# Kernel optimization log

Hardware: AMD Instinct MI355X
Metric: run time of the kernel (lower is better)

## Reference

```python
import math
import jax, jax.numpy as jnp
import numpy as np

N_EXPERTS = 8
CAP_FACTOR = 1.25
D_MODEL = 1024
D_FF = 4096
B, T = 8, 2048


def setup_inputs() -> dict:
    key = jax.random.key(0)
    k1, k2, k3, k4 = jax.random.split(key, 4)
    hidden = jax.random.normal(k1, (B, T, D_MODEL), dtype=jnp.float32)
    # router: Linear(d_model, n_experts, bias=False), init std=0.01; store as (D, E)
    router_w = jax.random.normal(k2, (D_MODEL, N_EXPERTS), dtype=jnp.float32) * 0.01
    # per-expert MLP weights stacked: W1 (E, D, F), W2 (E, F, D)
    s1 = 1.0 / math.sqrt(D_MODEL)
    s2 = 1.0 / math.sqrt(D_FF)
    W1 = jax.random.uniform(k3, (N_EXPERTS, D_MODEL, D_FF), dtype=jnp.float32, minval=-s1, maxval=s1)
    W2 = jax.random.uniform(k4, (N_EXPERTS, D_FF, D_MODEL), dtype=jnp.float32, minval=-s2, maxval=s2)
    return {"hidden": hidden, "router_w": router_w, "W1": W1, "W2": W2}


def reference(hidden, router_w, W1, W2):
    Bb, Tt, D = hidden.shape
    N = Bb * Tt
    E = router_w.shape[1]
    capacity = min(int(math.ceil(CAP_FACTOR * N / E)), N)

    hidden_flat = hidden.reshape(N, D)
    logits = hidden_flat @ router_w                 # (N, E)
    router_probs = jax.nn.softmax(logits, axis=-1)  # (N, E)

    scores = router_probs.T                         # (E, N)
    weights, indices = jax.lax.top_k(scores, capacity)  # (E, C) each

    # gather tokens per expert: (E, C, D)
    expert_in = hidden_flat[indices]
    h = jnp.einsum('ecd,edf->ecf', expert_in, W1)
    h = jax.nn.gelu(h, approximate=False)           # torch nn.GELU default (erf)
    expert_out = jnp.einsum('ecf,efd->ecd', h, W2)  # (E, C, D)
    contrib = weights[..., None] * expert_out       # (E, C, D)

    output = jnp.zeros((N, D), dtype=hidden.dtype)
    output = output.at[indices.reshape(-1)].add(contrib.reshape(-1, D))
    output = output.reshape(Bb, Tt, D)

    eps = 1e-8
    entropy = -(router_probs * jnp.log(router_probs + eps)).sum(-1)
    aux_loss = -entropy.mean()
    return output, aux_loss
```

## Files before the change

### kernel.cpp

```cpp
#include <hip/hip_runtime.h>
#include <hip/hip_bf16.h>
#include <math.h>

#define NTOK 16384
#define DM 1024
#define DFF 4096
#define NEXP 8
#define CAP 2560

typedef __bf16 bf16;
typedef float f32x4 __attribute__((ext_vector_type(4)));
typedef bf16 bf16x8 __attribute__((ext_vector_type(8)));
typedef bf16 bf16x4 __attribute__((ext_vector_type(4)));

#define OFF_PROBS 0ull
#define OFF_IDX   524288ull
#define OFF_WTS   606208ull
#define OFF_W1T   688128ull
#define OFF_W2T   67796992ull
#define OFF_X     134905856ull
#define OFF_ENT   OFF_X
#define OFF_H     176848896ull
#define WS_MIN    197820416ull
#define WS_FUSED  344621056ull

__device__ __forceinline__ void gl16(const bf16* g, const bf16* l) {
  __builtin_amdgcn_global_load_lds((const __attribute__((address_space(1))) void*)g,
                                   (__attribute__((address_space(3))) void*)l, 16, 0, 0);
}

__device__ __forceinline__ float gelu_f(float x) {
  float u = 1.5957691216057308f * (x + 0.044715f * x * x * x);
  return x * __builtin_amdgcn_rcpf(1.f + __expf(-u));
}

__global__ __launch_bounds__(256) void k_transpose_cvt(const float* __restrict__ src,
                                                       bf16* __restrict__ dst, int R, int C) {
  __shared__ float tile[64][69];
  int e = blockIdx.z;
  src += (size_t)e * R * C;
  dst += (size_t)e * R * C;
  int c0 = blockIdx.x * 64, r0 = blockIdx.y * 64;
  int t = threadIdx.x;
  int tr = t >> 4, tc4 = (t & 15) * 4;
#pragma unroll
  for (int i = 0; i < 4; i++) {
    int r = tr + i * 16;
    float4 v = *(const float4*)(src + (size_t)(r0 + r) * C + c0 + tc4);
    tile[r][tc4] = v.x; tile[r][tc4 + 1] = v.y; tile[r][tc4 + 2] = v.z; tile[r][tc4 + 3] = v.w;
  }
  __syncthreads();
#pragma unroll
  for (int i = 0; i < 4; i++) {
    int orr = tr + i * 16;
    bf16x4 o = {(bf16)tile[tc4][orr], (bf16)tile[tc4 + 1][orr],
                (bf16)tile[tc4 + 2][orr], (bf16)tile[tc4 + 3][orr]};
    *(bf16x4*)(dst + (size_t)(c0 + orr) * R + r0 + tc4) = o;
  }
}

__global__ __launch_bounds__(256) void k_router(const float* __restrict__ hidden,
                                                const float* __restrict__ rw,
                                                float* __restrict__ probsT,
                                                float* __restrict__ entPart) {
  __shared__ float went[4];
  int wv = threadIdx.x >> 6, lane = threadIdx.x & 63;
  int token = blockIdx.x * 4 + wv;
  float acc[NEXP];
#pragma unroll
  for (int e = 0; e < NEXP; e++) acc[e] = 0.f;
  const float* hp = hidden + (size_t)token * DM;
  for (int d = lane; d < DM; d += 64) {
    float h = hp[d];
#pragma unroll
    for (int e = 0; e < NEXP; e++) acc[e] = fmaf(h, rw[d * NEXP + e], acc[e]);
  }
#pragma unroll
  for (int e = 0; e < NEXP; e++) {
    float v = acc[e];
#pragma unroll
    for (int s = 1; s < 64; s <<= 1) v += __shfl_xor(v, s);
    acc[e] = v;
  }
  float mx = acc[0];
#pragma unroll
  for (int e = 1; e < NEXP; e++) mx = fmaxf(mx, acc[e]);
  float p[NEXP], s = 0.f;
#pragma unroll
  for (int e = 0; e < NEXP; e++) { p[e] = expf(acc[e] - mx); s += p[e]; }
  float inv = 1.f / s;
  float ent = 0.f;
#pragma unroll
  for (int e = 0; e < NEXP; e++) { p[e] *= inv; ent += p[e] * logf(p[e] + 1e-8f); }
  if (lane < NEXP) probsT[(size_t)lane * NTOK + token] = p[lane];
  if (lane == 0) went[wv] = ent;
  __syncthreads();
  if (threadIdx.x == 0) entPart[blockIdx.x] = went[0] + went[1] + went[2] + went[3];
}

__global__ __launch_bounds__(256) void k_aux(const float* __restrict__ part, float* __restrict__ outAux) {
  __shared__ float s[256];
  int t = threadIdx.x;
  float v = 0.f;
#pragma unroll
  for (int i = 0; i < 16; i++) v += part[i * 256 + t];
  s[t] = v;
  __syncthreads();
  for (int st = 128; st > 0; st >>= 1) {
    if (t < st) s[t] += s[t + st];
    __syncthreads();
  }
  if (t == 0) outAux[0] = s[0] * (1.f / (float)NTOK);
}

__global__ __launch_bounds__(1024) void k_topk(const float* __restrict__ probsT,
                                               int* __restrict__ idx,
                                               float* __restrict__ wts) {
  int e = blockIdx.x;
  const float* row = probsT + (size_t)e * NTOK;
  int t = threadIdx.x;
  unsigned u[16];
#pragma unroll
  for (int j = 0; j < 16; j++) u[j] = __float_as_uint(row[j * 1024 + t]);
  __shared__ int wred[16];
  __shared__ int bc;
  __shared__ int cnt_gt, cnt_eq;
  __shared__ int eqbuf[2048];
  int lane = t & 63, wv = t >> 6;
  unsigned prefix = 0;
  for (int bit = 30; bit >= 0; bit--) {
    unsigned cand = prefix | (1u << bit);
    int c = 0;
#pragma unroll
    for (int j = 0; j < 16; j++) c += (u[j] >= cand) ? 1 : 0;
#pragma unroll
    for (int s = 1; s < 64; s <<= 1) c += __shfl_xor(c, s);
    if (lane == 0) wred[wv] = c;
    __syncthreads();
    if (t == 0) { int tot = 0; for (int k = 0; k < 16; k++) tot += wred[k]; bc = tot; }
    __syncthreads();
    if (bc >= CAP) prefix = cand;
  }
  unsigned vC = prefix;
  if (t == 0) { cnt_gt = 0; cnt_eq = 0; }
  __syncthreads();
#pragma unroll
  for (int j = 0; j < 16; j++) {
    int i = j * 1024 + t;
    if (u[j] > vC) {
      int p = atomicAdd(&cnt_gt, 1);
      idx[e * CAP + p] = i;
      wts[e * CAP + p] = __uint_as_float(u[j]);
    } else if (u[j] == vC) {
      int p = atomicAdd(&cnt_eq, 1);
      if (p < 2048) eqbuf[p] = i;
    }
  }
  __syncthreads();
  int m = cnt_gt;
  int ne = cnt_eq > 2048 ? 2048 : cnt_eq;
  int needed = CAP - m;
  for (int j = t; j < ne; j += 1024) {
    int my = eqbuf[j];
    int rank = 0;
    for (int k = 0; k < ne; k++) rank += (eqbuf[k] < my) ? 1 : 0;
    if (rank < needed) {
      idx[e * CAP + m + rank] = my;
      wts[e * CAP + m + rank] = __uint_as_float(vC);
    }
  }
}

__global__ void k_gather(const float* __restrict__ hidden, const int* __restrict__ idx,
                         bf16* __restrict__ X) {
  int ec = blockIdx.x;
  int token = idx[ec];
  const float4* src = (const float4*)(hidden + (size_t)token * DM);
  bf16* dstrow = X + (size_t)ec * DM;
  int t = threadIdx.x;
  float4 v = src[t];
  bf16x4 o = {(bf16)v.x, (bf16)v.y, (bf16)v.z, (bf16)v.w};
  *(bf16x4*)(dstrow + t * 4) = o;
}

template <int EPI>
__global__ __launch_bounds__(256) void k_gemm128(
    const bf16* __restrict__ Ab, const bf16* __restrict__ Bb,
    bf16* __restrict__ Hb, const int* __restrict__ idxb, const float* __restrict__ wtsb,
    float* __restrict__ outb, int serialE) {
  constexpr int KD = (EPI == 0) ? DM : DFF;
  constexpr int NT = (EPI == 0) ? 16 : 32;

  __shared__ bf16 As[128 * 64];
  __shared__ bf16 Bs[128 * 64];

  int e, j;
  if (serialE >= 0) { e = serialE; j = blockIdx.x; }
  else { e = blockIdx.x & 7; j = blockIdx.x >> 3; }
  int bx = j % 20, jr = j / 20;
  int m0 = bx * 128, n0, k0;
  if constexpr (EPI == 0) { n0 = jr * 128; k0 = 0; }
  else { n0 = (jr & 7) * 128; k0 = (jr >> 3) * 2048; }

  const bf16* A = Ab + (size_t)e * ((size_t)CAP * KD) + (size_t)m0 * KD;
  const bf16* B = Bb + (size_t)e * ((size_t)DFF * DM) + (size_t)n0 * KD;

  int t = threadIdx.x, lane = t & 63, wv = t >> 6;
  int wm = wv >> 1, wn = wv & 1;
  int l3 = lane >> 3, l7 = lane & 7;
  int cswz = (l7 ^ l3) * 8;

  f32x4 acc[4][4];
#pragma unroll
  for (int m = 0; m < 4; m++)
#pragma unroll
    for (int n = 0; n < 4; n++) acc[m][n] = (f32x4){0.f, 0.f, 0.f, 0.f};

  const bf16* gA0 = A + (size_t)(wv * 32 + l3) * KD + cswz;
  const bf16* gB0 = B + (size_t)(wv * 32 + l3) * KD + cswz;
  bf16* lA0 = As + wv * 2048 + lane * 8;
  bf16* lB0 = Bs + wv * 2048 + lane * 8;

  for (int kt = 0; kt < NT; kt++) {
    int ke = k0 + kt * 64;
#pragma unroll
    for (int jj = 0; jj < 4; jj++) {
      gl16(gA0 + (size_t)jj * 8 * KD + ke, lA0 + jj * 512);
      gl16(gB0 + (size_t)jj * 8 * KD + ke, lB0 + jj * 512);
    }
    __syncthreads();
#pragma unroll
    for (int kk = 0; kk < 2; kk++) {
      int kslot = kk * 4 + (lane >> 4);
      int slt = (kslot ^ l7) * 16;
      bf16x8 af[4], bfm[4];
#pragma unroll
      for (int m = 0; m < 4; m++) {
        int rr = wm * 64 + m * 16 + (lane & 15);
        af[m] = *(const bf16x8*)((const char*)As + rr * 128 + slt);
      }
#pragma unroll
      for (int n = 0; n < 4; n++) {
        int rr = wn * 64 + n * 16 + (lane & 15);
        bfm[n] = *(const bf16x8*)((const char*)Bs + rr * 128 + slt);
      }
#pragma unroll
      for (int m = 0; m < 4; m++)
#pragma unroll
        for (int n = 0; n < 4; n++)
          acc[m][n] = __builtin_amdgcn_mfma_f32_16x16x32_bf16(af[m], bfm[n], acc[m][n], 0, 0, 0);
    }
    __syncthreads();
  }

  int cl = lane & 15, rg = (lane >> 4) * 4;
  if constexpr (EPI == 0) {
    bf16* He = Hb + (size_t)e * CAP * DFF;
#pragma unroll
    for (int m = 0; m < 4; m++) {
      int rowg = m0 + wm * 64 + m * 16 + rg;
#pragma unroll
      for (int n = 0; n < 4; n++) {
        int col = n0 + wn * 64 + n * 16 + cl;
#pragma unroll
        for (int rr = 0; rr < 4; rr++)
          He[(size_t)(rowg + rr) * DFF + col] = (bf16)gelu_f(acc[m][n][rr]);
      }
    }
  } else {
    const int* idxE = idxb + e * CAP;
    const float* wtsE = wtsb + e * CAP;
#pragma unroll
    for (int m = 0; m < 4; m++) {
      int rowg = m0 + wm * 64 + m * 16 + rg;
#pragma unroll
      for (int rr = 0; rr < 4; rr++) {
        int c = rowg + rr;
        int token = idxE[c];
        float w = wtsE[c];
        float* op = outb + (size_t)token * DM + n0 + wn * 64 + cl;
#pragma unroll
        for (int n = 0; n < 4; n++) atomicAdd(op + n * 16, w * acc[m][n][rr]);
      }
    }
  }
}

extern "C" void kernel_launch(void* const* d_in, const int* in_sizes, int n_in,
                              void* d_out, int out_size, void* d_ws, size_t ws_size,
                              hipStream_t stream) {
  const float* hidden = (const float*)d_in[0];
  const float* router_w = (const float*)d_in[1];
  const float* W1 = (const float*)d_in[2];
  const float* W2 = (const float*)d_in[3];
  float* out = (float*)d_out;
  if (ws_size < WS_MIN) return;

  char* ws = (char*)d_ws;
  float* probsT = (float*)(ws + OFF_PROBS);
  int* idxb = (int*)(ws + OFF_IDX);
  float* wtsb = (float*)(ws + OFF_WTS);
  bf16* W1T = (bf16*)(ws + OFF_W1T);
  bf16* W2T = (bf16*)(ws + OFF_W2T);
  bf16* Xall = (bf16*)(ws + OFF_X);
  float* entPart = (float*)(ws + OFF_ENT);
  bf16* Hbuf = (bf16*)(ws + OFF_H);

  hipMemsetAsync(d_out, 0, (size_t)out_size * sizeof(float), stream);

  k_transpose_cvt<<<dim3(DFF / 64, DM / 64, NEXP), 256, 0, stream>>>(W1, W1T, DM, DFF);
  k_transpose_cvt<<<dim3(DM / 64, DFF / 64, NEXP), 256, 0, stream>>>(W2, W2T, DFF, DM);

  k_router<<<NTOK / 4, 256, 0, stream>>>(hidden, router_w, probsT, entPart);
  k_aux<<<1, 256, 0, stream>>>(entPart, out + (size_t)NTOK * DM);
  k_topk<<<NEXP, 1024, 0, stream>>>(probsT, idxb, wtsb);
  k_gather<<<NEXP * CAP, 256, 0, stream>>>(hidden, idxb, Xall);

  if (ws_size >= WS_FUSED) {
    k_gemm128<0><<<NEXP * 20 * 32, 256, 0, stream>>>(Xall, W1T, Hbuf, nullptr, nullptr, nullptr, -1);
    k_gemm128<1><<<NEXP * 20 * 16, 256, 0, stream>>>(Hbuf, W2T, nullptr, idxb, wtsb, out, -1);
  } else {
    for (int e = 0; e < NEXP; e++) {
      bf16* Hadj = Hbuf - (size_t)e * CAP * DFF;
      k_gemm128<0><<<20 * 32, 256, 0, stream>>>(Xall, W1T, Hadj, nullptr, nullptr, nullptr, e);
      k_gemm128<1><<<20 * 16, 256, 0, stream>>>(Hadj, W2T, nullptr, idxb, wtsb, out, e);
    }
  }
}
```

Baseline: 661.6 us.

## Double-buffer second expert GEMM and drop split-K atomics

The second expert GEMM moves to a dedicated kernel that double-buffers LDS tiles, issuing the next tile's global-to-LDS loads before computing the current one and managing vmcnt/lgkmcnt waits explicitly. It also drops the split-K over DFF, so each block covers the full K=4096 and does half as many atomic adds to the output. The trade-off is half as many blocks (less parallelism), double the LDS use, which may lower occupancy, and a longer serial K loop per block.

After: 617.7 us. 6.6% less time.

```diff
diff --git a/kernel.cpp b/kernel.cpp
--- a/kernel.cpp
+++ b/kernel.cpp
@@ -27,6 +27,14 @@
 __device__ __forceinline__ void gl16(const bf16* g, const bf16* l) {
   __builtin_amdgcn_global_load_lds((const __attribute__((address_space(1))) void*)g,
                                    (__attribute__((address_space(3))) void*)l, 16, 0, 0);
+}
+
+__device__ __forceinline__ bf16x8 ldsrd16(const bf16* a) {
+  bf16x8 d;
+  asm volatile("ds_read_b128 %0, %1"
+               : "=v"(d)
+               : "v"((const __attribute__((address_space(3))) bf16*)a));
+  return d;
 }
 
 __device__ __forceinline__ float gelu_f(float x) {
@@ -183,13 +191,11 @@
   *(bf16x4*)(dstrow + t * 4) = o;
 }
 
-template <int EPI>
 __global__ __launch_bounds__(256) void k_gemm128(
     const bf16* __restrict__ Ab, const bf16* __restrict__ Bb,
-    bf16* __restrict__ Hb, const int* __restrict__ idxb, const float* __restrict__ wtsb,
-    float* __restrict__ outb, int serialE) {
-  constexpr int KD = (EPI == 0) ? DM : DFF;
-  constexpr int NT = (EPI == 0) ? 16 : 32;
+    bf16* __restrict__ Hb, int serialE) {
+  constexpr int KD = DM;
+  constexpr int NT = 16;
 
   __shared__ bf16 As[128 * 64];
   __shared__ bf16 Bs[128 * 64];
@@ -198,9 +204,7 @@
   if (serialE >= 0) { e = serialE; j = blockIdx.x; }
   else { e = blockIdx.x & 7; j = blockIdx.x >> 3; }
   int bx = j % 20, jr = j / 20;
-  int m0 = bx * 128, n0, k0;
-  if constexpr (EPI == 0) { n0 = jr * 128; k0 = 0; }
-  else { n0 = (jr & 7) * 128; k0 = (jr >> 3) * 2048; }
+  int m0 = bx * 128, n0 = jr * 128;
 
   const bf16* A = Ab + (size_t)e * ((size_t)CAP * KD) + (size_t)m0 * KD;
   const bf16* B = Bb + (size_t)e * ((size_t)DFF * DM) + (size_t)n0 * KD;
@@ -222,7 +226,7 @@
   bf16* lB0 = Bs + wv * 2048 + lane * 8;
 
   for (int kt = 0; kt < NT; kt++) {
-    int ke = k0 + kt * 64;
+    int ke = kt * 64;
 #pragma unroll
     for (int jj = 0; jj < 4; jj++) {
       gl16(gA0 + (size_t)jj * 8 * KD + ke, lA0 + jj * 512);
@@ -254,34 +258,118 @@
   }
 
   int cl = lane & 15, rg = (lane >> 4) * 4;
-  if constexpr (EPI == 0) {
-    bf16* He = Hb + (size_t)e * CAP * DFF;
-#pragma unroll
-    for (int m = 0; m < 4; m++) {
-      int rowg = m0 + wm * 64 + m * 16 + rg;
+  bf16* He = Hb + (size_t)e * CAP * DFF;
+#pragma unroll
+  for (int m = 0; m < 4; m++) {
+    int rowg = m0 + wm * 64 + m * 16 + rg;
+#pragma unroll
+    for (int n = 0; n < 4; n++) {
+      int col = n0 + wn * 64 + n * 16 + cl;
+#pragma unroll
+      for (int rr = 0; rr < 4; rr++)
+        He[(size_t)(rowg + rr) * DFF + col] = (bf16)gelu_f(acc[m][n][rr]);
+    }
+  }
+}
+
+__global__ __launch_bounds__(256) void k_gemm2ph(
+    const bf16* __restrict__ Hb, const bf16* __restrict__ Bb,
+    const int* __restrict__ idxb, const float* __restrict__ wtsb,
+    float* __restrict__ outb, int serialE) {
+  constexpr int KD = DFF;
+  constexpr int NT = 64;
+
+  __shared__ bf16 As[2][128 * 64];
+  __shared__ bf16 Bs[2][128 * 64];
+
+  int e, j;
+  if (serialE >= 0) { e = serialE; j = blockIdx.x; }
+  else { e = blockIdx.x & 7; j = blockIdx.x >> 3; }
+  int bx = j % 20, by = j / 20;
+  int m0 = bx * 128, n0 = by * 128;
+
+  const bf16* A = Hb + (size_t)e * CAP * DFF + (size_t)m0 * KD;
+  const bf16* B = Bb + (size_t)e * DM * DFF + (size_t)n0 * KD;
+
+  int t = threadIdx.x, lane = t & 63, wv = t >> 6;
+  int wm = wv >> 1, wn = wv & 1;
+  int l3 = lane >> 3, l7 = lane & 7;
+  int cswz = (l7 ^ l3) * 8;
+
+  const bf16* gA0 = A + (size_t)(wv * 32 + l3) * KD + cswz;
+  const bf16* gB0 = B + (size_t)(wv * 32 + l3) * KD + cswz;
+
+  f32x4 acc[4][4];
+#pragma unroll
+  for (int m = 0; m < 4; m++)
+#pragma unroll
+    for (int n = 0; n < 4; n++) acc[m][n] = (f32x4){0.f, 0.f, 0.f, 0.f};
+
+  auto STAGE = [&](int buf, int ke) {
+    bf16* lA = &As[buf][wv * 2048 + lane * 8];
+    bf16* lB = &Bs[buf][wv * 2048 + lane * 8];
+#pragma unroll
+    for (int jj = 0; jj < 4; jj++) {
+      gl16(gA0 + (size_t)jj * 8 * KD + ke, lA + jj * 512);
+      gl16(gB0 + (size_t)jj * 8 * KD + ke, lB + jj * 512);
+    }
+  };
+
+  STAGE(0, 0);
+
+  for (int kt = 0; kt < NT; kt++) {
+    int cur = kt & 1;
+    if (kt < NT - 1) {
+      STAGE(cur ^ 1, (kt + 1) * 64);
+      asm volatile("s_waitcnt vmcnt(8)");
+    } else {
+      asm volatile("s_waitcnt vmcnt(0)");
+    }
+    __builtin_amdgcn_s_barrier();
+
+    bf16x8 af[4][2], bfm[4][2];
+#pragma unroll
+    for (int kk = 0; kk < 2; kk++) {
+      int kslot = kk * 4 + (lane >> 4);
+      int slt = (kslot ^ l7) * 16;
+#pragma unroll
+      for (int m = 0; m < 4; m++) {
+        int rr = wm * 64 + m * 16 + (lane & 15);
+        af[m][kk] = ldsrd16((const bf16*)((const char*)&As[cur][0] + rr * 128 + slt));
+      }
 #pragma unroll
       for (int n = 0; n < 4; n++) {
-        int col = n0 + wn * 64 + n * 16 + cl;
-#pragma unroll
-        for (int rr = 0; rr < 4; rr++)
-          He[(size_t)(rowg + rr) * DFF + col] = (bf16)gelu_f(acc[m][n][rr]);
+        int rr = wn * 64 + n * 16 + (lane & 15);
+        bfm[n][kk] = ldsrd16((const bf16*)((const char*)&Bs[cur][0] + rr * 128 + slt));
       }
     }
-  } else {
-    const int* idxE = idxb + e * CAP;
-    const float* wtsE = wtsb + e * CAP;
-#pragma unroll
-    for (int m = 0; m < 4; m++) {
-      int rowg = m0 + wm * 64 + m * 16 + rg;
-#pragma unroll
-      for (int rr = 0; rr < 4; rr++) {
-        int c = rowg + rr;
-        int token = idxE[c];
-        float w = wtsE[c];
-        float* op = outb + (size_t)token * DM + n0 + wn * 64 + cl;
-#pragma unroll
-        for (int n = 0; n < 4; n++) atomicAdd(op + n * 16, w * acc[m][n][rr]);
-      }
+    asm volatile("s_waitcnt lgkmcnt(0)");
+    __builtin_amdgcn_sched_barrier(0);
+    __builtin_amdgcn_s_barrier();
+
+#pragma unroll
+    for (int kk = 0; kk < 2; kk++)
+#pragma unroll
+      for (int m = 0; m < 4; m++)
+#pragma unroll
+        for (int n = 0; n < 4; n++)
+          acc[m][n] = __builtin_amdgcn_mfma_f32_16x16x32_bf16(af[m][kk], bfm[n][kk], acc[m][n], 0, 0, 0);
+  }
+
+  int cl = lane & 15, rg = (lane >> 4) * 4;
+  const int* idxE = idxb + e * CAP;
+  const float* wtsE = wtsb + e * CAP;
+#pragma unroll
+  for (int m = 0; m < 4; m++) {
+    int rowg = m0 + wm * 64 + m * 16 + rg;
+#pragma unroll
+    for (int rr = 0; rr < 4; rr++) {
+      int c = rowg + rr;
+      int token = idxE[c];
+      float w = wtsE[c];
+      float* op = outb + (size_t)token * DM + n0 + wn * 64 + cl;
+#pragma unroll
+      for (int n = 0; n < 4; n++) atomicAdd(op + n * 16, w * acc[m][n][rr]);
     }
   }
 }
@@ -317,13 +405,13 @@
   k_gather<<<NEXP * CAP, 256, 0, stream>>>(hidden, idxb, Xall);
 
   if (ws_size >= WS_FUSED) {
-    k_gemm128<0><<<NEXP * 20 * 32, 256, 0, stream>>>(Xall, W1T, Hbuf, nullptr, nullptr, nullptr, -1);
-    k_gemm128<1><<<NEXP * 20 * 16, 256, 0, stream>>>(Hbuf, W2T, nullptr, idxb, wtsb, out, -1);
+    k_gemm128<<<NEXP * 20 * 32, 256, 0, stream>>>(Xall, W1T, Hbuf, -1);
+    k_gemm2ph<<<NEXP * 20 * 8, 256, 0, stream>>>(Hbuf, W2T, idxb, wtsb, out, -1);
   } else {
     for (int e = 0; e < NEXP; e++) {
       bf16* Hadj = Hbuf - (size_t)e * CAP * DFF;
-      k_gemm128<0><<<20 * 32, 256, 0, stream>>>(Xall, W1T, Hadj, nullptr, nullptr, nullptr, e);
-      k_gemm128<1><<<20 * 16, 256, 0, stream>>>(Hadj, W2T, nullptr, idxb, wtsb, out, e);
-    }
-  }
-}
+      k_gemm128<<<20 * 32, 256, 0, stream>>>(Xall, W1T, Hadj, e);
+      k_gemm2ph<<<20 * 8, 256, 0, stream>>>(Hadj, W2T, idxb, wtsb, out, e);
+    }
+  }
+}
```

## Rewrite expert GEMMs with 256-row tiles, double-buffered LDS and 512 threads

Applied to the files above, without the earlier changes.

Replaces the 128x128 single-buffered GEMM with a templated kernel using 256x256 (first GEMM) and 256x128 (second GEMM) tiles, 8 waves per block, and double-buffered LDS so global-to-LDS loads for the next k-step overlap MFMA work on the current one. LDS reads use inline ds_read_b128 with explicit waitcnt and sched_barrier to control instruction ordering. The second GEMM drops the split-K over DFF, so its atomics are no longer shared across two K halves, but it has far fewer blocks (640). The larger tiles raise register and LDS pressure (64 KB or 48 KB of LDS) and lower occupancy.

Result: faster. 590.6 us (-10.7%).

```diff
diff --git a/kernel.cpp b/kernel.cpp
--- a/kernel.cpp
+++ b/kernel.cpp
@@ -29,6 +29,14 @@
                                    (__attribute__((address_space(3))) void*)l, 16, 0, 0);
 }
 
+__device__ __forceinline__ bf16x8 ldsrd16(const bf16* a) {
+  bf16x8 d;
+  asm volatile("ds_read_b128 %0, %1"
+               : "=v"(d)
+               : "v"((const __attribute__((address_space(3))) bf16*)a));
+  return d;
+}
+
 __device__ __forceinline__ float gelu_f(float x) {
   float u = 1.5957691216057308f * (x + 0.044715f * x * x * x);
   return x * __builtin_amdgcn_rcpf(1.f + __expf(-u));
@@ -183,85 +191,134 @@
   *(bf16x4*)(dstrow + t * 4) = o;
 }
 
-template <int EPI>
-__global__ __launch_bounds__(256) void k_gemm128(
+template <int EPI, int BM, int BN, int WMW, int WNW, int NT, int KD>
+__global__ __launch_bounds__(512) void k_gemm2ph(
     const bf16* __restrict__ Ab, const bf16* __restrict__ Bb,
     bf16* __restrict__ Hb, const int* __restrict__ idxb, const float* __restrict__ wtsb,
     float* __restrict__ outb, int serialE) {
-  constexpr int KD = (EPI == 0) ? DM : DFF;
-  constexpr int NT = (EPI == 0) ? 16 : 32;
-
-  __shared__ bf16 As[128 * 64];
-  __shared__ bf16 Bs[128 * 64];
+  constexpr int MF = (BM / WMW) / 16;
+  constexpr int NF = (BN / WNW) / 16;
+  constexpr int CA = BM / 8;
+  constexpr int CB = BN / 8;
+  constexpr int S = (CA + CB) / 8;
+  constexpr bool SPLIT = (MF + NF) <= 8;
+
+  __shared__ bf16 As[2][BM * 64];
+  __shared__ bf16 Bs[2][BN * 64];
 
   int e, j;
   if (serialE >= 0) { e = serialE; j = blockIdx.x; }
   else { e = blockIdx.x & 7; j = blockIdx.x >> 3; }
-  int bx = j % 20, jr = j / 20;
-  int m0 = bx * 128, n0, k0;
-  if constexpr (EPI == 0) { n0 = jr * 128; k0 = 0; }
-  else { n0 = (jr & 7) * 128; k0 = (jr >> 3) * 2048; }
-
-  const bf16* A = Ab + (size_t)e * ((size_t)CAP * KD) + (size_t)m0 * KD;
-  const bf16* B = Bb + (size_t)e * ((size_t)DFF * DM) + (size_t)n0 * KD;
+  int m0 = (j % 10) * 256;
+  int n0 = (j / 10) * BN;
+
+  const bf16* A = Ab + (size_t)e * CAP * KD + (size_t)m0 * KD;
+  const bf16* B = Bb + (size_t)e * DFF * DM + (size_t)n0 * KD;
 
   int t = threadIdx.x, lane = t & 63, wv = t >> 6;
-  int wm = wv >> 1, wn = wv & 1;
-  int l3 = lane >> 3, l7 = lane & 7;
+  int wm = wv / WNW, wn = wv % WNW;
+  int l3 = lane >> 3, l7 = lane & 7, l15 = lane & 15, khalf = lane >> 4;
   int cswz = (l7 ^ l3) * 8;
 
-  f32x4 acc[4][4];
-#pragma unroll
-  for (int m = 0; m < 4; m++)
-#pragma unroll
-    for (int n = 0; n < 4; n++) acc[m][n] = (f32x4){0.f, 0.f, 0.f, 0.f};
-
-  const bf16* gA0 = A + (size_t)(wv * 32 + l3) * KD + cswz;
-  const bf16* gB0 = B + (size_t)(wv * 32 + l3) * KD + cswz;
-  bf16* lA0 = As + wv * 2048 + lane * 8;
-  bf16* lB0 = Bs + wv * 2048 + lane * 8;
+  const bf16* gA0 = A + (size_t)l3 * KD + cswz;
+  const bf16* gB0 = B + (size_t)l3 * KD + cswz;
+
+  f32x4 acc[MF][NF];
+#pragma unroll
+  for (int m = 0; m < MF; m++)
+#pragma unroll
+    for (int n = 0; n < NF; n++) acc[m][n] = (f32x4){0.f, 0.f, 0.f, 0.f};
+
+  auto STAGE = [&](int buf, int ke) {
+#pragma unroll
+    for (int s = 0; s < S; s++) {
+      int c = wv + s * 8;
+      if (c < CA) gl16(gA0 + (size_t)(c * 8) * KD + ke, &As[buf][c * 512 + lane * 8]);
+      else gl16(gB0 + (size_t)((c - CA) * 8) * KD + ke, &Bs[buf][(c - CA) * 512 + lane * 8]);
+    }
+  };
+
+  STAGE(0, 0);
+
+  int rowA = wm * (BM / WMW) + l15;
+  int rowB = wn * (BN / WNW) + l15;
 
   for (int kt = 0; kt < NT; kt++) {
-    int ke = k0 + kt * 64;
-#pragma unroll
-    for (int jj = 0; jj < 4; jj++) {
-      gl16(gA0 + (size_t)jj * 8 * KD + ke, lA0 + jj * 512);
-      gl16(gB0 + (size_t)jj * 8 * KD + ke, lB0 + jj * 512);
-    }
-    __syncthreads();
-#pragma unroll
-    for (int kk = 0; kk < 2; kk++) {
-      int kslot = kk * 4 + (lane >> 4);
-      int slt = (kslot ^ l7) * 16;
-      bf16x8 af[4], bfm[4];
-#pragma unroll
-      for (int m = 0; m < 4; m++) {
-        int rr = wm * 64 + m * 16 + (lane & 15);
-        af[m] = *(const bf16x8*)((const char*)As + rr * 128 + slt);
-      }
-#pragma unroll
-      for (int n = 0; n < 4; n++) {
-        int rr = wn * 64 + n * 16 + (lane & 15);
-        bfm[n] = *(const bf16x8*)((const char*)Bs + rr * 128 + slt);
-      }
-#pragma unroll
-      for (int m = 0; m < 4; m++)
-#pragma unroll
-        for (int n = 0; n < 4; n++)
-          acc[m][n] = __builtin_amdgcn_mfma_f32_16x16x32_bf16(af[m], bfm[n], acc[m][n], 0, 0, 0);
-    }
-    __syncthreads();
+    int cur = kt & 1;
+    if (kt < NT - 1) {
+      STAGE(cur ^ 1, (kt + 1) * 64);
+      asm volatile("s_waitcnt vmcnt(%0)" :: "n"(S));
+    } else {
+      asm volatile("s_waitcnt vmcnt(0)");
+    }
+    __builtin_amdgcn_s_barrier();
+
+    const char* Ap = (const char*)&As[cur][0];
+    const char* Bp = (const char*)&Bs[cur][0];
+    int slt0 = ((0 + khalf) ^ l7) * 16;
+    int slt1 = ((4 + khalf) ^ l7) * 16;
+    bf16x8 aF[MF][2], bF[NF][2];
+
+    if constexpr (SPLIT) {
+#pragma unroll
+      for (int m = 0; m < MF; m++) aF[m][0] = ldsrd16((const bf16*)(Ap + (rowA + m * 16) * 128 + slt0));
+#pragma unroll
+      for (int n = 0; n < NF; n++) bF[n][0] = ldsrd16((const bf16*)(Bp + (rowB + n * 16) * 128 + slt0));
+#pragma unroll
+      for (int m = 0; m < MF; m++) aF[m][1] = ldsrd16((const bf16*)(Ap + (rowA + m * 16) * 128 + slt1));
+#pragma unroll
+      for (int n = 0; n < NF; n++) bF[n][1] = ldsrd16((const bf16*)(Bp + (rowB + n * 16) * 128 + slt1));
+      asm volatile("s_waitcnt lgkmcnt(%0)" :: "n"(MF + NF));
+      __builtin_amdgcn_sched_barrier(0);
+#pragma unroll
+      for (int m = 0; m < MF; m++)
+#pragma unroll
+        for (int n = 0; n < NF; n++)
+          acc[m][n] = __builtin_amdgcn_mfma_f32_16x16x32_bf16(aF[m][0], bF[n][0], acc[m][n], 0, 0, 0);
+      asm volatile("s_waitcnt lgkmcnt(0)");
+      __builtin_amdgcn_sched_barrier(0);
+      __builtin_amdgcn_s_barrier();
+#pragma unroll
+      for (int m = 0; m < MF; m++)
+#pragma unroll
+        for (int n = 0; n < NF; n++)
+          acc[m][n] = __builtin_amdgcn_mfma_f32_16x16x32_bf16(aF[m][1], bF[n][1], acc[m][n], 0, 0, 0);
+    } else {
+#pragma unroll
+      for (int m = 0; m < MF; m++) aF[m][0] = ldsrd16((const bf16*)(Ap + (rowA + m * 16) * 128 + slt0));
+#pragma unroll
+      for (int n = 0; n < NF; n++) bF[n][0] = ldsrd16((const bf16*)(Bp + (rowB + n * 16) * 128 + slt0));
+      asm volatile("s_waitcnt lgkmcnt(0)");
+      __builtin_amdgcn_sched_barrier(0);
+#pragma unroll
+      for (int m = 0; m < MF; m++)
+#pragma unroll
+        for (int n = 0; n < NF; n++)
+          acc[m][n] = __builtin_amdgcn_mfma_f32_16x16x32_bf16(aF[m][0], bF[n][0], acc[m][n], 0, 0, 0);
+#pragma unroll
+      for (int m = 0; m < MF; m++) aF[m][1] = ldsrd16((const bf16*)(Ap + (rowA + m * 16) * 128 + slt1));
+#pragma unroll
+      for (int n = 0; n < NF; n++) bF[n][1] = ldsrd16((const bf16*)(Bp + (rowB + n * 16) * 128 + slt1));
+      asm volatile("s_waitcnt lgkmcnt(0)");
+      __builtin_amdgcn_sched_barrier(0);
+      __builtin_amdgcn_s_barrier();
+#pragma unroll
+      for (int m = 0; m < MF; m++)
+#pragma unroll
+        for (int n = 0; n < NF; n++)
+          acc[m][n] = __builtin_amdgcn_mfma_f32_16x16x32_bf16(aF[m][1], bF[n][1], acc[m][n], 0, 0, 0);
+    }
   }
 
   int cl = lane & 15, rg = (lane >> 4) * 4;
   if constexpr (EPI == 0) {
     bf16* He = Hb + (size_t)e * CAP * DFF;
 #pragma unroll
-    for (int m = 0; m < 4; m++) {
-      int rowg = m0 + wm * 64 + m * 16 + rg;
-#pragma unroll
-      for (int n = 0; n < 4; n++) {
-        int col = n0 + wn * 64 + n * 16 + cl;
+    for (int m = 0; m < MF; m++) {
+      int rowg = m0 + wm * (BM / WMW) + m * 16 + rg;
+#pragma unroll
+      for (int n = 0; n < NF; n++) {
+        int col = n0 + wn * (BN / WNW) + n * 16 + cl;
 #pragma unroll
         for (int rr = 0; rr < 4; rr++)
           He[(size_t)(rowg + rr) * DFF + col] = (bf16)gelu_f(acc[m][n][rr]);
@@ -271,16 +328,16 @@
     const int* idxE = idxb + e * CAP;
     const float* wtsE = wtsb + e * CAP;
 #pragma unroll
-    for (int m = 0; m < 4; m++) {
-      int rowg = m0 + wm * 64 + m * 16 + rg;
+    for (int m = 0; m < MF; m++) {
+      int rowg = m0 + wm * (BM / WMW) + m * 16 + rg;
 #pragma unroll
       for (int rr = 0; rr < 4; rr++) {
         int c = rowg + rr;
         int token = idxE[c];
         float w = wtsE[c];
-        float* op = outb + (size_t)token * DM + n0 + wn * 64 + cl;
-#pragma unroll
-        for (int n = 0; n < 4; n++) atomicAdd(op + n * 16, w * acc[m][n][rr]);
+        float* op = outb + (size_t)token * DM + n0 + wn * (BN / WNW) + cl;
+#pragma unroll
+        for (int n = 0; n < NF; n++) atomicAdd(op + n * 16, w * acc[m][n][rr]);
       }
     }
   }
@@ -317,13 +374,17 @@
   k_gather<<<NEXP * CAP, 256, 0, stream>>>(hidden, idxb, Xall);
 
   if (ws_size >= WS_FUSED) {
-    k_gemm128<0><<<NEXP * 20 * 32, 256, 0, stream>>>(Xall, W1T, Hbuf, nullptr, nullptr, nullptr, -1);
-    k_gemm128<1><<<NEXP * 20 * 16, 256, 0, stream>>>(Hbuf, W2T, nullptr, idxb, wtsb, out, -1);
+    k_gemm2ph<0, 256, 256, 2, 4, 16, DM><<<NEXP * 160, 512, 0, stream>>>(
+        Xall, W1T, Hbuf, nullptr, nullptr, nullptr, -1);
+    k_gemm2ph<1, 256, 128, 4, 2, 64, DFF><<<NEXP * 80, 512, 0, stream>>>(
+        Hbuf, W2T, nullptr, idxb, wtsb, out, -1);
   } else {
     for (int e = 0; e < NEXP; e++) {
       bf16* Hadj = Hbuf - (size_t)e * CAP * DFF;
-      k_gemm128<0><<<20 * 32, 256, 0, stream>>>(Xall, W1T, Hadj, nullptr, nullptr, nullptr, e);
-      k_gemm128<1><<<20 * 16, 256, 0, stream>>>(Hadj, W2T, nullptr, idxb, wtsb, out, e);
-    }
-  }
-}
+      k_gemm2ph<0, 256, 256, 2, 4, 16, DM><<<160, 512, 0, stream>>>(
+          Xall, W1T, Hadj, nullptr, nullptr, nullptr, e);
+      k_gemm2ph<1, 256, 128, 4, 2, 64, DFF><<<80, 512, 0, stream>>>(
+          Hadj, W2T, nullptr, idxb, wtsb, out, e);
+    }
+  }
+}
```
